# Kernel optimization log

Hardware: AMD Instinct MI355X
Metric: run time of the kernel (lower is better)

Reference implementation:

```python
import jax, jax.numpy as jnp
import numpy as np

D_MODEL = 2048
EXPAND = 2
D_INNER = EXPAND * D_MODEL   # 4096
D_STATE = 128
D_CONV = 4
HEADDIM = 64
NHEADS = D_INNER // HEADDIM  # 64
NGROUPS = 1
CONV_DIM = D_INNER + 2 * NGROUPS * D_STATE           # 4352
D_IN_PROJ = 2 * D_INNER + 2 * NGROUPS * D_STATE + NHEADS  # 8512
B, T = 2, 2048
EPS = 1e-5


def setup_inputs() -> dict:
    key = jax.random.key(0)
    ks = jax.random.split(key, 12)
    x = jax.random.normal(ks[0], (B, T, D_MODEL), dtype=jnp.float32)
    cos = jax.random.normal(ks[1], (T, HEADDIM), dtype=jnp.float32)
    sin = jax.random.normal(ks[2], (T, HEADDIM), dtype=jnp.float32)
    in_proj_w = jax.random.normal(ks[3], (D_IN_PROJ, D_MODEL), dtype=jnp.float32) * 0.02
    conv_w = jax.random.normal(ks[4], (CONV_DIM, D_CONV), dtype=jnp.float32) * 0.2
    conv_b = jnp.zeros((CONV_DIM,), dtype=jnp.float32)
    # dt_bias = softplus^{-1}(dt) for dt ~ U[0.001, 0.1]
    dt = jax.random.uniform(ks[5], (NHEADS,), minval=0.001, maxval=0.1)
    dt_bias = (jnp.log(jnp.expm1(dt))).astype(jnp.float32)
    A_log = jnp.log(jax.random.uniform(ks[6], (NHEADS,), minval=1.0, maxval=16.0)).astype(jnp.float32)
    Dskip = jnp.ones((NHEADS,), dtype=jnp.float32)
    norm_w = jnp.ones((D_INNER,), dtype=jnp.float32)
    out_proj_w = jax.random.normal(ks[7], (D_MODEL, D_INNER), dtype=jnp.float32) * 0.02
    return {"x": x, "cos": cos, "sin": sin, "in_proj_w": in_proj_w,
            "conv_w": conv_w, "conv_b": conv_b, "dt_bias": dt_bias,
            "A_log": A_log, "Dskip": Dskip, "norm_w": norm_w,
            "out_proj_w": out_proj_w}


def _mamba2_fwd(x, in_proj_w, conv_w, conv_b, dt_bias, A_log, Dskip, norm_w, out_proj_w):
    # in_proj -> [z, xBC, dt]
    zxbcdt = jnp.einsum('btd,ed->bte', x, in_proj_w)  # [B,T,8512]
    z = zxbcdt[..., :D_INNER]
    xBC = zxbcdt[..., D_INNER:D_INNER + CONV_DIM]
    dt_raw = zxbcdt[..., D_INNER + CONV_DIM:]          # [B,T,H]

    # depthwise causal conv1d + SiLU
    xBC_pad = jnp.pad(xBC, ((0, 0), (D_CONV - 1, 0), (0, 0)))
    conv = conv_b
    for k in range(D_CONV):
        conv = conv + xBC_pad[:, k:k + T, :] * conv_w[:, k]
    xBC = jax.nn.silu(conv)

    x_ssm = xBC[..., :D_INNER].reshape(x.shape[0], T, NHEADS, HEADDIM)  # [B,T,H,P]
    Bmat = xBC[..., D_INNER:D_INNER + D_STATE]                          # [B,T,N] (ngroups=1)
    Cmat = xBC[..., D_INNER + D_STATE:]                                 # [B,T,N]

    dt = jax.nn.softplus(dt_raw + dt_bias)   # [B,T,H]
    A = -jnp.exp(A_log)                      # [H]
    dA = jnp.exp(dt * A)                     # [B,T,H], in (0,1]
    dtx = dt[..., None] * x_ssm              # [B,T,H,P]

    # selective scan over time (state h: [B,H,P,N])
    def step(h, xs_t):
        dA_t, dtx_t, B_t, C_t = xs_t  # [B,H],[B,H,P],[B,N],[B,N]
        h = h * dA_t[:, :, None, None] + dtx_t[:, :, :, None] * B_t[:, None, None, :]
        y = jnp.einsum('bhpn,bn->bhp', h, C_t)
        return h, y

    h0 = jnp.zeros((x.shape[0], NHEADS, HEADDIM, D_STATE), dtype=x.dtype)
    xs = (jnp.swapaxes(dA, 0, 1), jnp.swapaxes(dtx, 0, 1),
          jnp.swapaxes(Bmat, 0, 1), jnp.swapaxes(Cmat, 0, 1))
    _, ys = jax.lax.scan(step, h0, xs)       # ys: [T,B,H,P]
    y = jnp.swapaxes(ys, 0, 1) + Dskip[None, None, :, None] * x_ssm  # [B,T,H,P]
    y = y.reshape(x.shape[0], T, D_INNER)

    # gated RMSNorm: gate first, then normalize
    y = y * jax.nn.silu(z)
    y = y * jax.lax.rsqrt(jnp.mean(jnp.square(y), axis=-1, keepdims=True) + EPS) * norm_w

    return jnp.einsum('bte,de->btd', y, out_proj_w)  # [B,T,D]


def reference(x, cos, sin, in_proj_w, conv_w, conv_b, dt_bias, A_log, Dskip, norm_w, out_proj_w):
    # cos/sin accepted but ignored (Mamba needs no positional encoding)
    return _mamba2_fwd(x, in_proj_w, conv_w, conv_b, dt_bias, A_log, Dskip, norm_w, out_proj_w)
```

## Files before the change

### kernel.cpp

```cpp
#include <hip/hip_runtime.h>

#define D_MODEL 2048
#define D_INNER 4096
#define D_STATE 128
#define HEADDIM 64
#define NHEADS 64
#define CONV_DIM 4352
#define D_IN_PROJ 8512
#define BB 2
#define TSEQ 2048
#define BT (BB*TSEQ)
#define NCHUNK 32
#define LCH 64
#define EPS_F 1e-5f

typedef __bf16 bf16x8 __attribute__((ext_vector_type(8)));
typedef float f32x4 __attribute__((ext_vector_type(4)));

__device__ __forceinline__ float bf2f(unsigned short u){
  unsigned int x = ((unsigned int)u) << 16;
  return __builtin_bit_cast(float, x);
}
__device__ __forceinline__ unsigned short f2bf(float f){
  unsigned int x = __builtin_bit_cast(unsigned int, f);
  x += 0x7fffu + ((x >> 16) & 1u);
  return (unsigned short)(x >> 16);
}

__device__ __forceinline__ void async_copy16(const unsigned short* g, unsigned short* l) {
  __builtin_amdgcn_global_load_lds(
      (const __attribute__((address_space(1))) unsigned int*)g,
      (__attribute__((address_space(3))) unsigned int*)l, 16, 0, 0);
}

__global__ __launch_bounds__(256) void cast_kernel(
    const float* __restrict__ in, unsigned short* __restrict__ out, int n)
{
  int i = (blockIdx.x * 256 + threadIdx.x) * 8;
  if (i >= n) return;
  float4 a = *(const float4*)&in[i];
  float4 b = *(const float4*)&in[i + 4];
  unsigned short o[8] = { f2bf(a.x), f2bf(a.y), f2bf(a.z), f2bf(a.w),
                          f2bf(b.x), f2bf(b.y), f2bf(b.z), f2bf(b.w) };
  *(uint4*)&out[i] = *(uint4*)o;
}

template <bool F32OUT>
__global__ __launch_bounds__(256) void gemm_tn_kernel(
    const unsigned short* __restrict__ A, const unsigned short* __restrict__ Bm,
    void* __restrict__ Cout, int M, int N, int K, int NT, int MT)
{
  __shared__ __align__(16) unsigned short As[128 * 64];
  __shared__ __align__(16) unsigned short Bs[128 * 64];
  int tid = threadIdx.x;

  int bid = blockIdx.x;
  int fullBands = NT >> 3;
  int blocksFull = fullBands * 8 * MT;
  int mt, nt;
  if (bid < blocksFull) {
    int band = bid / (8 * MT);
    int wI = bid - band * (8 * MT);
    nt = band * 8 + (wI & 7);
    mt = wI >> 3;
  } else {
    int rem = bid - blocksFull;
    int WL = NT - fullBands * 8;
    nt = fullBands * 8 + rem % WL;
    mt = rem / WL;
  }
  int m0 = mt * 128, n0 = nt * 128;

  int wave = tid >> 6, lane = tid & 63;
  int wm = wave >> 1, wn = wave & 1;
  int lm = lane & 15, kqb = lane >> 4;
  int sw = lm & 7;

  int lr = lane >> 3, lc = lane & 7, bg = lc ^ lr;
  const unsigned short* Ap = A + (size_t)(m0 + wave * 32 + lr) * K + bg * 8;
  const unsigned short* Bp = Bm + (size_t)(n0 + wave * 32 + lr) * K + bg * 8;

  f32x4 acc[4][4] = {};

  for (int k0 = 0; k0 < K; k0 += 64) {
#pragma unroll
    for (int q = 0; q < 4; q++) {
      async_copy16(Ap + (size_t)q * 8 * K + k0, &As[(wave * 32 + q * 8) * 64]);
      async_copy16(Bp + (size_t)q * 8 * K + k0, &Bs[(wave * 32 + q * 8) * 64]);
    }
    __syncthreads();
#pragma unroll
    for (int kk = 0; kk < 64; kk += 32) {
      int b0 = (kk >> 3) + kqb;
      int boff = (b0 ^ sw) * 8;
      bf16x8 af[4], bfr[4];
#pragma unroll
      for (int i = 0; i < 4; i++) af[i]  = *(const bf16x8*)&As[(wm * 64 + i * 16 + lm) * 64 + boff];
#pragma unroll
      for (int j = 0; j < 4; j++) bfr[j] = *(const bf16x8*)&Bs[(wn * 64 + j * 16 + lm) * 64 + boff];
#pragma unroll
      for (int i = 0; i < 4; i++)
#pragma unroll
        for (int j = 0; j < 4; j++)
          acc[i][j] = __builtin_amdgcn_mfma_f32_16x16x32_bf16(af[i], bfr[j], acc[i][j], 0, 0, 0);
    }
    __syncthreads();
  }

  int rq = lane >> 4;
#pragma unroll
  for (int i = 0; i < 4; i++) {
#pragma unroll
    for (int j = 0; j < 4; j++) {
      int col = n0 + wn * 64 + j * 16 + lm;
      if (col < N) {
        int mrow = m0 + wm * 64 + i * 16 + rq * 4;
#pragma unroll
        for (int r = 0; r < 4; r++) {
          if (F32OUT) ((float*)Cout)[(size_t)(mrow + r) * N + col] = acc[i][j][r];
          else ((unsigned short*)Cout)[(size_t)(mrow + r) * N + col] = f2bf(acc[i][j][r]);
        }
      }
    }
  }
}

__global__ __launch_bounds__(256) void conv_silu_kernel(
    const unsigned short* __restrict__ zx, const float* __restrict__ conv_w,
    const float* __restrict__ conv_b,
    unsigned short* __restrict__ xconv, float* __restrict__ Bf, float* __restrict__ Cf)
{
  const int NG = CONV_DIM / 8;
  int gid = blockIdx.x * 256 + threadIdx.x;
  if (gid >= BT * NG) return;
  int cg = gid % NG; int bt = gid / NG;
  int t = bt % TSEQ;
  int c0 = cg * 8;

  float wgt[8][4];
#pragma unroll
  for (int i = 0; i < 8; i++)
#pragma unroll
    for (int k = 0; k < 4; k++) wgt[i][k] = conv_w[(c0 + i) * 4 + k];

  float acc[8];
#pragma unroll
  for (int i = 0; i < 8; i++) acc[i] = conv_b[c0 + i];

#pragma unroll
  for (int k = 0; k < 4; k++) {
    int ts = t - 3 + k;
    if (ts < 0) continue;
    unsigned short xv[8];
    *(uint4*)xv = *(const uint4*)&zx[(size_t)(bt - 3 + k) * D_IN_PROJ + D_INNER + c0];
#pragma unroll
    for (int i = 0; i < 8; i++) acc[i] = fmaf(bf2f(xv[i]), wgt[i][k], acc[i]);
  }

  if (c0 < D_INNER) {
    unsigned short o[8];
#pragma unroll
    for (int i = 0; i < 8; i++) { float v = acc[i]; v = v / (1.f + expf(-v)); o[i] = f2bf(v); }
    *(uint4*)&xconv[(size_t)bt * D_INNER + c0] = *(uint4*)o;
  } else if (c0 < D_INNER + D_STATE) {
    int n = c0 - D_INNER;
#pragma unroll
    for (int i = 0; i < 8; i++) { float v = acc[i]; Bf[(size_t)bt * D_STATE + n + i] = v / (1.f + expf(-v)); }
  } else {
    int n = c0 - D_INNER - D_STATE;
#pragma unroll
    for (int i = 0; i < 8; i++) { float v = acc[i]; Cf[(size_t)bt * D_STATE + n + i] = v / (1.f + expf(-v)); }
  }
}

__global__ __launch_bounds__(256) void dt_prep_kernel(
    const unsigned short* __restrict__ zx, const float* __restrict__ dt_bias,
    const float* __restrict__ A_log, float* __restrict__ dtv, float* __restrict__ lav)
{
  int gid = blockIdx.x * 256 + threadIdx.x;
  int h = gid & 63; int bt = gid >> 6;
  float x = bf2f(zx[(size_t)bt * D_IN_PROJ + D_INNER + CONV_DIM + h]) + dt_bias[h];
  float dt = (x > 20.f) ? x : log1pf(expf(x));
  float A = -expf(A_log[h]);
  dtv[gid] = dt;
  lav[gid] = dt * A;
}

__global__ __launch_bounds__(256) void cumsum_kernel(
    const float* __restrict__ lav, float* __restrict__ ca)
{
  int g = blockIdx.x * 4 + (threadIdx.x >> 6);
  int lane = threadIdx.x & 63;
  int h = g & 63; int cb = g >> 6;
  float v = lav[((size_t)cb * 64 + lane) * 64 + h];
#pragma unroll
  for (int off = 1; off < 64; off <<= 1) {
    float t = __shfl_up(v, off);
    if (lane >= off) v += t;
  }
  ca[(size_t)g * 64 + lane] = v;
}

__global__ __launch_bounds__(256) void chunk_g_kernel(
    const float* __restrict__ Bf, const float* __restrict__ Cf,
    unsigned short* __restrict__ G)
{
  __shared__ __align__(16) unsigned short Cs[64][136];
  __shared__ __align__(16) unsigned short Bs2[64][136];
  int tid = threadIdx.x; int cb = blockIdx.x;
  size_t bt0 = (size_t)cb * 64;
  int row = tid >> 2, seg = (tid & 3) * 32;
#pragma unroll
  for (int u = 0; u < 32; u += 8) {
    float4 a = *(const float4*)&Cf[(bt0 + row) * 128 + seg + u];
    float4 b = *(const float4*)&Cf[(bt0 + row) * 128 + seg + u + 4];
    unsigned short o[8] = { f2bf(a.x), f2bf(a.y), f2bf(a.z), f2bf(a.w),
                            f2bf(b.x), f2bf(b.y), f2bf(b.z), f2bf(b.w) };
    *(uint4*)&Cs[row][seg + u] = *(uint4*)o;
    float4 c = *(const float4*)&Bf[(bt0 + row) * 128 + seg + u];
    float4 d = *(const float4*)&Bf[(bt0 + row) * 128 + seg + u + 4];
    unsigned short o2[8] = { f2bf(c.x), f2bf(c.y), f2bf(c.z), f2bf(c.w),
                             f2bf(d.x), f2bf(d.y), f2bf(d.z), f2bf(d.w) };
    *(uint4*)&Bs2[row][seg + u] = *(uint4*)o2;
  }
  __syncthreads();
  int wave = tid >> 6, lane = tid & 63, lm = lane & 15, kq = (lane >> 4) * 8, rq = lane >> 4;
  f32x4 acc[4] = {};
#pragma unroll
  for (int ks = 0; ks < 4; ks++) {
    bf16x8 af = *(const bf16x8*)&Cs[wave * 16 + lm][ks * 32 + kq];
#pragma unroll
    for (int jt = 0; jt < 4; jt++) {
      bf16x8 bb = *(const bf16x8*)&Bs2[jt * 16 + lm][ks * 32 + kq];
      acc[jt] = __builtin_amdgcn_mfma_f32_16x16x32_bf16(af, bb, acc[jt], 0, 0, 0);
    }
  }
#pragma unroll
  for (int jt = 0; jt < 4; jt++)
#pragma unroll
    for (int r = 0; r < 4; r++) {
      int i = wave * 16 + rq * 4 + r, j = jt * 16 + lm;
      G[(size_t)cb * 4096 + i * 64 + j] = f2bf(acc[jt][r]);
    }
}

__global__ __launch_bounds__(256) void chunk_state_kernel(
    const float* __restrict__ Bf, const unsigned short* __restrict__ xconv,
    const float* __restrict__ dtv, const float* __restrict__ ca,
    unsigned short* __restrict__ S)
{
  __shared__ __align__(16) unsigned short Ax[64][72];
  __shared__ __align__(16) unsigned short Bn[128][72];
  int tid = threadIdx.x;
  int c = blockIdx.x & 31, h = (blockIdx.x >> 5) & 63, b = blockIdx.x >> 11;
  int cb = b * 32 + c;
  size_t bt0 = (size_t)cb * 64;
  const float* cag = &ca[((size_t)cb * 64 + h) * 64];
  float ca63 = cag[63];
  {
    int j = tid >> 2, pseg = (tid & 3) * 16;
    float wj = expf(ca63 - cag[j]) * dtv[(bt0 + j) * 64 + h];
    unsigned short xv[16];
    *(uint4*)&xv[0] = *(const uint4*)&xconv[(bt0 + j) * 4096 + h * 64 + pseg];
    *(uint4*)&xv[8] = *(const uint4*)&xconv[(bt0 + j) * 4096 + h * 64 + pseg + 8];
#pragma unroll
    for (int q = 0; q < 16; q++) Ax[pseg + q][j] = f2bf(wj * bf2f(xv[q]));
  }
  {
    int j = tid >> 2, nseg = (tid & 3) * 32;
#pragma unroll
    for (int u = 0; u < 32; u += 4) {
      float4 bv = *(const float4*)&Bf[(bt0 + j) * 128 + nseg + u];
      Bn[nseg + u][j] = f2bf(bv.x); Bn[nseg + u + 1][j] = f2bf(bv.y);
      Bn[nseg + u + 2][j] = f2bf(bv.z); Bn[nseg + u + 3][j] = f2bf(bv.w);
    }
  }
  __syncthreads();
  int wave = tid >> 6, lane = tid & 63, lm = lane & 15, kq = (lane >> 4) * 8, rq = lane >> 4;
  f32x4 acc[8] = {};
#pragma unroll
  for (int ks = 0; ks < 2; ks++) {
    bf16x8 af = *(const bf16x8*)&Ax[wave * 16 + lm][ks * 32 + kq];
#pragma unroll
    for (int nt = 0; nt < 8; nt++) {
      bf16x8 bb = *(const bf16x8*)&Bn[nt * 16 + lm][ks * 32 + kq];
      acc[nt] = __builtin_amdgcn_mfma_f32_16x16x32_bf16(af, bb, acc[nt], 0, 0, 0);
    }
  }
  size_t sbase = ((size_t)(b * 64 + h) * 32 + c) * 8192;
#pragma unroll
  for (int nt = 0; nt < 8; nt++)
#pragma unroll
    for (int r = 0; r < 4; r++) {
      int p = wave * 16 + rq * 4 + r, n = nt * 16 + lm;
      S[sbase + p * 128 + n] = f2bf(acc[nt][r]);
    }
}

__global__ __launch_bounds__(256) void state_pass_kernel(
    unsigned short* __restrict__ Shin, const float* __restrict__ ca)
{
  int part = blockIdx.x & 7, bh = blockIdx.x >> 3;
  int h = bh & 63, b = bh >> 6;
  int e0 = part * 1024 + threadIdx.x * 4;
  size_t base = (size_t)bh * 32 * 8192;
  float hc[4] = {0.f, 0.f, 0.f, 0.f};
  for (int c = 0; c < 32; c++) {
    float sc = expf(ca[(((size_t)(b * 32 + c)) * 64 + h) * 64 + 63]);
    size_t off = base + (size_t)c * 8192 + e0;
    uint2 sv = *(uint2*)&Shin[off];
    unsigned short* sp = (unsigned short*)&sv;
    unsigned short ho[4];
#pragma unroll
    for (int q = 0; q < 4; q++) ho[q] = f2bf(hc[q]);
    *(uint2*)&Shin[off] = *(uint2*)ho;
#pragma unroll
    for (int q = 0; q < 4; q++) hc[q] = sc * hc[q] + bf2f(sp[q]);
  }
}

__global__ __launch_bounds__(256) void chunk_y_kernel(
    const unsigned short* __restrict__ G, const float* __restrict__ Cf,
    const unsigned short* __restrict__ xconv, const float* __restrict__ dtv,
    const float* __restrict__ ca, const unsigned short* __restrict__ hin,
    const float* __restrict__ Dskip, unsigned short* __restrict__ yp)
{
  __shared__ __align__(16) unsigned short Aop[64][200];
  __shared__ __align__(16) unsigned short Bop[64][200];
  __shared__ __align__(16) unsigned short xs[64][72];
  __shared__ float cas[64]; __shared__ float dts[64];
  int tid = threadIdx.x;
  int c = blockIdx.x & 31, h = (blockIdx.x >> 5) & 63, b = blockIdx.x >> 11;
  int cb = b * 32 + c;
  size_t bt0 = (size_t)cb * 64;
  if (tid < 64) {
    cas[tid] = ca[((size_t)cb * 64 + h) * 64 + tid];
    dts[tid] = dtv[(bt0 + tid) * 64 + h];
  }
  __syncthreads();
  {
    int i = tid >> 2, jseg = (tid & 3) * 16;
    float cai = cas[i];
    unsigned short gv[16];
    *(uint4*)&gv[0] = *(const uint4*)&G[(size_t)cb * 4096 + i * 64 + jseg];
    *(uint4*)&gv[8] = *(const uint4*)&G[(size_t)cb * 4096 + i * 64 + jseg + 8];
    unsigned short o[16];
#pragma unroll
    for (int q = 0; q < 16; q++) {
      int j = jseg + q;
      float m = (j <= i) ? bf2f(gv[q]) * expf(cai - cas[j]) : 0.f;
      o[q] = f2bf(m);
    }
    *(uint4*)&Aop[i][jseg] = *(uint4*)&o[0];
    *(uint4*)&Aop[i][jseg + 8] = *(uint4*)&o[8];
  }
  {
    int i = tid >> 2, nseg = (tid & 3) * 32;
    float sci = expf(cas[i]);
#pragma unroll
    for (int u = 0; u < 32; u += 8) {
      float4 a = *(const float4*)&Cf[(bt0 + i) * 128 + nseg + u];
      float4 bq = *(const float4*)&Cf[(bt0 + i) * 128 + nseg + u + 4];
      unsigned short o[8] = { f2bf(sci * a.x), f2bf(sci * a.y), f2bf(sci * a.z), f2bf(sci * a.w),
                              f2bf(sci * bq.x), f2bf(sci * bq.y), f2bf(sci * bq.z), f2bf(sci * bq.w) };
      *(uint4*)&Aop[i][64 + nseg + u] = *(uint4*)o;
    }
  }
  {
    int j = tid >> 2, pseg = (tid & 3) * 16;
    float dtj = dts[j];
    unsigned short xv[16];
    *(uint4*)&xv[0] = *(const uint4*)&xconv[(bt0 + j) * 4096 + h * 64 + pseg];
    *(uint4*)&xv[8] = *(const uint4*)&xconv[(bt0 + j) * 4096 + h * 64 + pseg + 8];
#pragma unroll
    for (int q = 0; q < 16; q++) Bop[pseg + q][j] = f2bf(dtj * bf2f(xv[q]));
    *(uint4*)&xs[j][pseg] = *(uint4*)&xv[0];
    *(uint4*)&xs[j][pseg + 8] = *(uint4*)&xv[8];
  }
  {
    int p = tid >> 2, nseg = (tid & 3) * 32;
    size_t hb = ((size_t)(b * 64 + h) * 32 + c) * 8192 + p * 128 + nseg;
#pragma unroll
    for (int u = 0; u < 32; u += 8)
      *(uint4*)&Bop[p][64 + nseg + u] = *(const uint4*)&hin[hb + u];
  }
  __syncthreads();
  int wave = tid >> 6, lane = tid & 63, lm = lane & 15, kq = (lane >> 4) * 8, rq = lane >> 4;
  f32x4 acc[4] = {};
#pragma unroll
  for (int ks = 0; ks < 6; ks++) {
    bf16x8 af = *(const bf16x8*)&Aop[wave * 16 + lm][ks * 32 + kq];
#pragma unroll
    for (int pt = 0; pt < 4; pt++) {
      bf16x8 bb = *(const bf16x8*)&Bop[pt * 16 + lm][ks * 32 + kq];
      acc[pt] = __builtin_amdgcn_mfma_f32_16x16x32_bf16(af, bb, acc[pt], 0, 0, 0);
    }
  }
  float dsk = Dskip[h];
#pragma unroll
  for (int pt = 0; pt < 4; pt++)
#pragma unroll
    for (int r = 0; r < 4; r++) {
      int i = wave * 16 + rq * 4 + r, p = pt * 16 + lm;
      float y = acc[pt][r] + dsk * bf2f(xs[i][p]);
      yp[(bt0 + i) * 4096 + h * 64 + p] = f2bf(y);
    }
}

__global__ __launch_bounds__(256) void gate_norm_kernel(
    const unsigned short* __restrict__ yp, const unsigned short* __restrict__ zx,
    const float* __restrict__ norm_w, unsigned short* __restrict__ ybf)
{
  int row = blockIdx.x; int tid = threadIdx.x;
  int c0 = tid * 16;
  unsigned short y0[16], zv[16];
  const size_t base = (size_t)row * D_INNER + c0;
  *(uint4*)&y0[0] = *(const uint4*)&yp[base];
  *(uint4*)&y0[8] = *(const uint4*)&yp[base + 8];
  const size_t zbase = (size_t)row * D_IN_PROJ + c0;
  *(uint4*)&zv[0] = *(const uint4*)&zx[zbase];
  *(uint4*)&zv[8] = *(const uint4*)&zx[zbase + 8];

  float g[16]; float ss = 0.f;
#pragma unroll
  for (int i = 0; i < 16; i++) {
    float y = bf2f(y0[i]);
    float z = bf2f(zv[i]);
    float gate = z / (1.f + expf(-z));
    float gv = y * gate;
    g[i] = gv; ss += gv * gv;
  }
#pragma unroll
  for (int o = 32; o >= 1; o >>= 1) ss += __shfl_xor(ss, o);
  __shared__ float red[4]; __shared__ float stot;
  if ((tid & 63) == 0) red[tid >> 6] = ss;
  __syncthreads();
  if (tid == 0) stot = red[0] + red[1] + red[2] + red[3];
  __syncthreads();
  float scale = rsqrtf(stot * (1.f / D_INNER) + EPS_F);
  unsigned short o16[16];
#pragma unroll
  for (int i = 0; i < 16; i++) o16[i] = f2bf(g[i] * scale * norm_w[c0 + i]);
  *(uint4*)&ybf[base] = *(uint4*)&o16[0];
  *(uint4*)&ybf[base + 8] = *(uint4*)&o16[8];
}

extern "C" void kernel_launch(void* const* d_in, const int* in_sizes, int n_in,
                              void* d_out, int out_size, void* d_ws, size_t ws_size,
                              hipStream_t stream) {
  (void)in_sizes; (void)n_in; (void)out_size; (void)ws_size;
  const float* x          = (const float*)d_in[0];
  const float* in_proj_w  = (const float*)d_in[3];
  const float* conv_w     = (const float*)d_in[4];
  const float* conv_b     = (const float*)d_in[5];
  const float* dt_bias    = (const float*)d_in[6];
  const float* A_log      = (const float*)d_in[7];
  const float* Dskip      = (const float*)d_in[8];
  const float* norm_w     = (const float*)d_in[9];
  const float* out_proj_w = (const float*)d_in[10];
  float* out = (float*)d_out;

  char* w = (char*)d_ws;
  unsigned short* zx    = (unsigned short*)(w);
  unsigned short* xconv = (unsigned short*)(w + 69730304);
  float* Bf  = (float*)(w + 103284736);
  float* Cf  = (float*)(w + 105381888);
  float* dtv = (float*)(w + 107479040);
  float* lav = (float*)(w + 108527616);
  float* ca  = (float*)(w + 109576192);
  unsigned short* G    = (unsigned short*)(w + 110624768);
  unsigned short* Shin = (unsigned short*)(w + 111149056);
  unsigned short* yp   = (unsigned short*)(w + 178257920);
  unsigned short* xb   = (unsigned short*)(w + 111149056);
  unsigned short* wib  = (unsigned short*)(w + 127926272);
  unsigned short* ybf  = (unsigned short*)(w + 111149056);
  unsigned short* wob  = (unsigned short*)(w + 144703488);

  cast_kernel<<<BT * D_MODEL / 8 / 256, 256, 0, stream>>>(x, xb, BT * D_MODEL);
  cast_kernel<<<D_IN_PROJ * D_MODEL / 8 / 256, 256, 0, stream>>>(in_proj_w, wib, D_IN_PROJ * D_MODEL);
  {
    int NT = (D_IN_PROJ + 127) / 128, MT = BT / 128;
    gemm_tn_kernel<false><<<NT * MT, 256, 0, stream>>>(
        xb, wib, zx, BT, D_IN_PROJ, D_MODEL, NT, MT);
  }
  conv_silu_kernel<<<(BT * (CONV_DIM / 8) + 255) / 256, 256, 0, stream>>>(
      zx, conv_w, conv_b, xconv, Bf, Cf);
  dt_prep_kernel<<<(BT * NHEADS) / 256, 256, 0, stream>>>(zx, dt_bias, A_log, dtv, lav);
  cumsum_kernel<<<BB * NCHUNK * NHEADS / 4, 256, 0, stream>>>(lav, ca);
  chunk_g_kernel<<<BB * NCHUNK, 256, 0, stream>>>(Bf, Cf, G);
  chunk_state_kernel<<<BB * NHEADS * NCHUNK, 256, 0, stream>>>(Bf, xconv, dtv, ca, Shin);
  state_pass_kernel<<<BB * NHEADS * 8, 256, 0, stream>>>(Shin, ca);
  chunk_y_kernel<<<BB * NHEADS * NCHUNK, 256, 0, stream>>>(G, Cf, xconv, dtv, ca, Shin, Dskip, yp);
  gate_norm_kernel<<<BT, 256, 0, stream>>>(yp, zx, norm_w, ybf);
  cast_kernel<<<D_MODEL * D_INNER / 8 / 256, 256, 0, stream>>>(out_proj_w, wob, D_MODEL * D_INNER);
  {
    int NT = D_MODEL / 128, MT = BT / 128;
    gemm_tn_kernel<true><<<NT * MT, 256, 0, stream>>>(
        ybf, wob, out, BT, D_MODEL, D_INNER, NT, MT);
  }
}
```

Baseline: 614.4 us.

## Store B/C as bf16, fuse dt prep into cumsum, batch heads in chunk_state

```diff
diff --git a/kernel.cpp b/kernel.cpp
--- a/kernel.cpp
+++ b/kernel.cpp
@@ -127,8 +127,8 @@
 
 __global__ __launch_bounds__(256) void conv_silu_kernel(
     const unsigned short* __restrict__ zx, const float* __restrict__ conv_w,
-    const float* __restrict__ conv_b,
-    unsigned short* __restrict__ xconv, float* __restrict__ Bf, float* __restrict__ Cf)
+    const float* __restrict__ conv_b, unsigned short* __restrict__ xconv,
+    unsigned short* __restrict__ Bbf, unsigned short* __restrict__ Cbf)
 {
   const int NG = CONV_DIM / 8;
   int gid = blockIdx.x * 256 + threadIdx.x;
@@ -157,52 +157,40 @@
     for (int i = 0; i < 8; i++) acc[i] = fmaf(bf2f(xv[i]), wgt[i][k], acc[i]);
   }
 
+  unsigned short o[8];
+#pragma unroll
+  for (int i = 0; i < 8; i++) { float v = acc[i]; o[i] = f2bf(v / (1.f + expf(-v))); }
   if (c0 < D_INNER) {
-    unsigned short o[8];
-#pragma unroll
-    for (int i = 0; i < 8; i++) { float v = acc[i]; v = v / (1.f + expf(-v)); o[i] = f2bf(v); }
     *(uint4*)&xconv[(size_t)bt * D_INNER + c0] = *(uint4*)o;
   } else if (c0 < D_INNER + D_STATE) {
-    int n = c0 - D_INNER;
-#pragma unroll
-    for (int i = 0; i < 8; i++) { float v = acc[i]; Bf[(size_t)bt * D_STATE + n + i] = v / (1.f + expf(-v)); }
+    *(uint4*)&Bbf[(size_t)bt * D_STATE + (c0 - D_INNER)] = *(uint4*)o;
   } else {
-    int n = c0 - D_INNER - D_STATE;
-#pragma unroll
-    for (int i = 0; i < 8; i++) { float v = acc[i]; Cf[(size_t)bt * D_STATE + n + i] = v / (1.f + expf(-v)); }
-  }
-}
-
-__global__ __launch_bounds__(256) void dt_prep_kernel(
+    *(uint4*)&Cbf[(size_t)bt * D_STATE + (c0 - D_INNER - D_STATE)] = *(uint4*)o;
+  }
+}
+
+__global__ __launch_bounds__(256) void dtcum_kernel(
     const unsigned short* __restrict__ zx, const float* __restrict__ dt_bias,
-    const float* __restrict__ A_log, float* __restrict__ dtv, float* __restrict__ lav)
-{
-  int gid = blockIdx.x * 256 + threadIdx.x;
-  int h = gid & 63; int bt = gid >> 6;
-  float x = bf2f(zx[(size_t)bt * D_IN_PROJ + D_INNER + CONV_DIM + h]) + dt_bias[h];
-  float dt = (x > 20.f) ? x : log1pf(expf(x));
-  float A = -expf(A_log[h]);
-  dtv[gid] = dt;
-  lav[gid] = dt * A;
-}
-
-__global__ __launch_bounds__(256) void cumsum_kernel(
-    const float* __restrict__ lav, float* __restrict__ ca)
+    const float* __restrict__ A_log, float* __restrict__ dtv, float* __restrict__ ca)
 {
   int g = blockIdx.x * 4 + (threadIdx.x >> 6);
   int lane = threadIdx.x & 63;
   int h = g & 63; int cb = g >> 6;
-  float v = lav[((size_t)cb * 64 + lane) * 64 + h];
+  size_t bt = (size_t)cb * 64 + lane;
+  float xr = bf2f(zx[bt * D_IN_PROJ + D_INNER + CONV_DIM + h]) + dt_bias[h];
+  float dt = (xr > 20.f) ? xr : log1pf(expf(xr));
+  float v = dt * (-expf(A_log[h]));
 #pragma unroll
   for (int off = 1; off < 64; off <<= 1) {
     float t = __shfl_up(v, off);
     if (lane >= off) v += t;
   }
+  dtv[bt * NHEADS + h] = dt;
   ca[(size_t)g * 64 + lane] = v;
 }
 
 __global__ __launch_bounds__(256) void chunk_g_kernel(
-    const float* __restrict__ Bf, const float* __restrict__ Cf,
+    const unsigned short* __restrict__ Bbf, const unsigned short* __restrict__ Cbf,
     unsigned short* __restrict__ G)
 {
   __shared__ __align__(16) unsigned short Cs[64][136];
@@ -212,16 +200,8 @@
   int row = tid >> 2, seg = (tid & 3) * 32;
 #pragma unroll
   for (int u = 0; u < 32; u += 8) {
-    float4 a = *(const float4*)&Cf[(bt0 + row) * 128 + seg + u];
-    float4 b = *(const float4*)&Cf[(bt0 + row) * 128 + seg + u + 4];
-    unsigned short o[8] = { f2bf(a.x), f2bf(a.y), f2bf(a.z), f2bf(a.w),
-                            f2bf(b.x), f2bf(b.y), f2bf(b.z), f2bf(b.w) };
-    *(uint4*)&Cs[row][seg + u] = *(uint4*)o;
-    float4 c = *(const float4*)&Bf[(bt0 + row) * 128 + seg + u];
-    float4 d = *(const float4*)&Bf[(bt0 + row) * 128 + seg + u + 4];
-    unsigned short o2[8] = { f2bf(c.x), f2bf(c.y), f2bf(c.z), f2bf(c.w),
-                             f2bf(d.x), f2bf(d.y), f2bf(d.z), f2bf(d.w) };
-    *(uint4*)&Bs2[row][seg + u] = *(uint4*)o2;
+    *(uint4*)&Cs[row][seg + u]  = *(const uint4*)&Cbf[(bt0 + row) * 128 + seg + u];
+    *(uint4*)&Bs2[row][seg + u] = *(const uint4*)&Bbf[(bt0 + row) * 128 + seg + u];
   }
   __syncthreads();
   int wave = tid >> 6, lane = tid & 63, lm = lane & 15, kq = (lane >> 4) * 8, rq = lane >> 4;
@@ -245,56 +225,57 @@
 }
 
 __global__ __launch_bounds__(256) void chunk_state_kernel(
-    const float* __restrict__ Bf, const unsigned short* __restrict__ xconv,
+    const unsigned short* __restrict__ Bbf, const unsigned short* __restrict__ xconv,
     const float* __restrict__ dtv, const float* __restrict__ ca,
     unsigned short* __restrict__ S)
 {
   __shared__ __align__(16) unsigned short Ax[64][72];
   __shared__ __align__(16) unsigned short Bn[128][72];
   int tid = threadIdx.x;
-  int c = blockIdx.x & 31, h = (blockIdx.x >> 5) & 63, b = blockIdx.x >> 11;
+  int c = blockIdx.x & 31, hb = (blockIdx.x >> 5) & 15, b = blockIdx.x >> 9;
   int cb = b * 32 + c;
   size_t bt0 = (size_t)cb * 64;
-  const float* cag = &ca[((size_t)cb * 64 + h) * 64];
-  float ca63 = cag[63];
-  {
-    int j = tid >> 2, pseg = (tid & 3) * 16;
-    float wj = expf(ca63 - cag[j]) * dtv[(bt0 + j) * 64 + h];
+  {
+    int j = tid >> 2, nseg = (tid & 3) * 32;
+    unsigned short bv[32];
+#pragma unroll
+    for (int u = 0; u < 32; u += 8)
+      *(uint4*)&bv[u] = *(const uint4*)&Bbf[(bt0 + j) * 128 + nseg + u];
+#pragma unroll
+    for (int u = 0; u < 32; u++) Bn[nseg + u][j] = bv[u];
+  }
+  int wave = tid >> 6, lane = tid & 63, lm = lane & 15, kq = (lane >> 4) * 8, rq = lane >> 4;
+  int j = tid >> 2, pseg = (tid & 3) * 16;
+  for (int hh = 0; hh < 4; hh++) {
+    int h = hb * 4 + hh;
+    const float* cag = &ca[((size_t)cb * 64 + h) * 64];
+    float wj = expf(cag[63] - cag[j]) * dtv[(bt0 + j) * 64 + h];
     unsigned short xv[16];
     *(uint4*)&xv[0] = *(const uint4*)&xconv[(bt0 + j) * 4096 + h * 64 + pseg];
     *(uint4*)&xv[8] = *(const uint4*)&xconv[(bt0 + j) * 4096 + h * 64 + pseg + 8];
+    if (hh) __syncthreads();
 #pragma unroll
     for (int q = 0; q < 16; q++) Ax[pseg + q][j] = f2bf(wj * bf2f(xv[q]));
-  }
-  {
-    int j = tid >> 2, nseg = (tid & 3) * 32;
-#pragma unroll
-    for (int u = 0; u < 32; u += 4) {
-      float4 bv = *(const float4*)&Bf[(bt0 + j) * 128 + nseg + u];
-      Bn[nseg + u][j] = f2bf(bv.x); Bn[nseg + u + 1][j] = f2bf(bv.y);
-      Bn[nseg + u + 2][j] = f2bf(bv.z); Bn[nseg + u + 3][j] = f2bf(bv.w);
-    }
-  }
-  __syncthreads();
-  int wave = tid >> 6, lane = tid & 63, lm = lane & 15, kq = (lane >> 4) * 8, rq = lane >> 4;
-  f32x4 acc[8] = {};
-#pragma unroll
-  for (int ks = 0; ks < 2; ks++) {
-    bf16x8 af = *(const bf16x8*)&Ax[wave * 16 + lm][ks * 32 + kq];
-#pragma unroll
-    for (int nt = 0; nt < 8; nt++) {
-      bf16x8 bb = *(const bf16x8*)&Bn[nt * 16 + lm][ks * 32 + kq];
-      acc[nt] = __builtin_amdgcn_mfma_f32_16x16x32_bf16(af, bb, acc[nt], 0, 0, 0);
-    }
-  }
-  size_t sbase = ((size_t)(b * 64 + h) * 32 + c) * 8192;
-#pragma unroll
-  for (int nt = 0; nt < 8; nt++)
-#pragma unroll
-    for (int r = 0; r < 4; r++) {
-      int p = wave * 16 + rq * 4 + r, n = nt * 16 + lm;
-      S[sbase + p * 128 + n] = f2bf(acc[nt][r]);
-    }
+    __syncthreads();
+    f32x4 acc[8] = {};
+#pragma unroll
+    for (int ks = 0; ks < 2; ks++) {
+      bf16x8 af = *(const bf16x8*)&Ax[wave * 16 + lm][ks * 32 + kq];
+#pragma unroll
+      for (int nt = 0; nt < 8; nt++) {
+        bf16x8 bb = *(const bf16x8*)&Bn[nt * 16 + lm][ks * 32 + kq];
+        acc[nt] = __builtin_amdgcn_mfma_f32_16x16x32_bf16(af, bb, acc[nt], 0, 0, 0);
+      }
+    }
+    size_t sbase = ((size_t)(b * 64 + h) * 32 + c) * 8192;
+#pragma unroll
+    for (int nt = 0; nt < 8; nt++)
+#pragma unroll
+      for (int r = 0; r < 4; r++) {
+        int p = wave * 16 + rq * 4 + r, n = nt * 16 + lm;
+        S[sbase + p * 128 + n] = f2bf(acc[nt][r]);
+      }
+  }
 }
 
 __global__ __launch_bounds__(256) void state_pass_kernel(
@@ -320,14 +301,13 @@
 }
 
 __global__ __launch_bounds__(256) void chunk_y_kernel(
-    const unsigned short* __restrict__ G, const float* __restrict__ Cf,
+    const unsigned short* __restrict__ G, const unsigned short* __restrict__ Cbf,
     const unsigned short* __restrict__ xconv, const float* __restrict__ dtv,
     const float* __restrict__ ca, const unsigned short* __restrict__ hin,
     const float* __restrict__ Dskip, unsigned short* __restrict__ yp)
 {
   __shared__ __align__(16) unsigned short Aop[64][200];
   __shared__ __align__(16) unsigned short Bop[64][200];
-  __shared__ __align__(16) unsigned short xs[64][72];
   __shared__ float cas[64]; __shared__ float dts[64];
   int tid = threadIdx.x;
   int c = blockIdx.x & 31, h = (blockIdx.x >> 5) & 63, b = blockIdx.x >> 11;
@@ -348,7 +328,7 @@
 #pragma unroll
     for (int q = 0; q < 16; q++) {
       int j = jseg + q;
-      float m = (j <= i) ? bf2f(gv[q]) * expf(cai - cas[j]) : 0.f;
+      float m = (j <= i) ? bf2f(gv[q]) * expf(cai - cas[j]) * dts[j] : 0.f;
       o[q] = f2bf(m);
     }
     *(uint4*)&Aop[i][jseg] = *(uint4*)&o[0];
@@ -359,23 +339,21 @@
     float sci = expf(cas[i]);
 #pragma unroll
     for (int u = 0; u < 32; u += 8) {
-      float4 a = *(const float4*)&Cf[(bt0 + i) * 128 + nseg + u];
-      float4 bq = *(const float4*)&Cf[(bt0 + i) * 128 + nseg + u + 4];
-      unsigned short o[8] = { f2bf(sci * a.x), f2bf(sci * a.y), f2bf(sci * a.z), f2bf(sci * a.w),
-                              f2bf(sci * bq.x), f2bf(sci * bq.y), f2bf(sci * bq.z), f2bf(sci * bq.w) };
+      unsigned short cv[8];
+      *(uint4*)cv = *(const uint4*)&Cbf[(bt0 + i) * 128 + nseg + u];
+      unsigned short o[8];
+#pragma unroll
+      for (int q = 0; q < 8; q++) o[q] = f2bf(sci * bf2f(cv[q]));
       *(uint4*)&Aop[i][64 + nseg + u] = *(uint4*)o;
     }
   }
   {
     int j = tid >> 2, pseg = (tid & 3) * 16;
-    float dtj = dts[j];
     unsigned short xv[16];
     *(uint4*)&xv[0] = *(const uint4*)&xconv[(bt0 + j) * 4096 + h * 64 + pseg];
     *(uint4*)&xv[8] = *(const uint4*)&xconv[(bt0 + j) * 4096 + h * 64 + pseg + 8];
 #pragma unroll
-    for (int q = 0; q < 16; q++) Bop[pseg + q][j] = f2bf(dtj * bf2f(xv[q]));
-    *(uint4*)&xs[j][pseg] = *(uint4*)&xv[0];
-    *(uint4*)&xs[j][pseg + 8] = *(uint4*)&xv[8];
+    for (int q = 0; q < 16; q++) Bop[pseg + q][j] = xv[q];
   }
   {
     int p = tid >> 2, nseg = (tid & 3) * 32;
@@ -402,7 +380,7 @@
 #pragma unroll
     for (int r = 0; r < 4; r++) {
       int i = wave * 16 + rq * 4 + r, p = pt * 16 + lm;
-      float y = acc[pt][r] + dsk * bf2f(xs[i][p]);
+      float y = acc[pt][r] + dsk * bf2f(Bop[p][i]);
       yp[(bt0 + i) * 4096 + h * 64 + p] = f2bf(y);
     }
 }
@@ -463,10 +441,9 @@
   char* w = (char*)d_ws;
   unsigned short* zx    = (unsigned short*)(w);
   unsigned short* xconv = (unsigned short*)(w + 69730304);
-  float* Bf  = (float*)(w + 103284736);
-  float* Cf  = (float*)(w + 105381888);
+  unsigned short* Bbf = (unsigned short*)(w + 103284736);
+  unsigned short* Cbf = (unsigned short*)(w + 105381888);
   float* dtv = (float*)(w + 107479040);
-  float* lav = (float*)(w + 108527616);
   float* ca  = (float*)(w + 109576192);
   unsigned short* G    = (unsigned short*)(w + 110624768);
   unsigned short* Shin = (unsigned short*)(w + 111149056);
@@ -484,13 +461,12 @@
         xb, wib, zx, BT, D_IN_PROJ, D_MODEL, NT, MT);
   }
   conv_silu_kernel<<<(BT * (CONV_DIM / 8) + 255) / 256, 256, 0, stream>>>(
-      zx, conv_w, conv_b, xconv, Bf, Cf);
-  dt_prep_kernel<<<(BT * NHEADS) / 256, 256, 0, stream>>>(zx, dt_bias, A_log, dtv, lav);
-  cumsum_kernel<<<BB * NCHUNK * NHEADS / 4, 256, 0, stream>>>(lav, ca);
-  chunk_g_kernel<<<BB * NCHUNK, 256, 0, stream>>>(Bf, Cf, G);
-  chunk_state_kernel<<<BB * NHEADS * NCHUNK, 256, 0, stream>>>(Bf, xconv, dtv, ca, Shin);
+      zx, conv_w, conv_b, xconv, Bbf, Cbf);
+  dtcum_kernel<<<BB * NCHUNK * NHEADS / 4, 256, 0, stream>>>(zx, dt_bias, A_log, dtv, ca);
+  chunk_g_kernel<<<BB * NCHUNK, 256, 0, stream>>>(Bbf, Cbf, G);
+  chunk_state_kernel<<<BB * 16 * NCHUNK, 256, 0, stream>>>(Bbf, xconv, dtv, ca, Shin);
   state_pass_kernel<<<BB * NHEADS * 8, 256, 0, stream>>>(Shin, ca);
-  chunk_y_kernel<<<BB * NHEADS * NCHUNK, 256, 0, stream>>>(G, Cf, xconv, dtv, ca, Shin, Dskip, yp);
+  chunk_y_kernel<<<BB * NHEADS * NCHUNK, 256, 0, stream>>>(G, Cbf, xconv, dtv, ca, Shin, Dskip, yp);
   gate_norm_kernel<<<BT, 256, 0, stream>>>(yp, zx, norm_w, ybf);
   cast_kernel<<<D_MODEL * D_INNER / 8 / 256, 256, 0, stream>>>(out_proj_w, wob, D_MODEL * D_INNER);
   {
```

Result: no change. 602.8 us (-1.9%).
